# Performance work log

Measured on AMD Instinct MI355X. Metric: run time of the kernel, lower is better.

Reference implementation:

```python
import jax, jax.numpy as jnp
import numpy as np

N, D, E = 100000, 128, 800000

def setup_inputs() -> dict:
    key = jax.random.key(0)
    k1, k2, k3, k4 = jax.random.split(key, 4)
    z = jax.random.normal(k1, (N, D), dtype=jnp.float32)
    edge_index = jax.random.randint(k2, (2, E), 0, N, dtype=jnp.int64)
    # PyTorch-style init scale for Linear layers (kaiming-uniform-ish via normal is fine for a numeric reference)
    W1 = jax.random.normal(k3, (2 * D, D), dtype=jnp.float32) * (1.0 / np.sqrt(2 * D))
    b1 = jnp.zeros((D,), dtype=jnp.float32)
    W2 = jax.random.normal(k4, (D, 1), dtype=jnp.float32) * (1.0 / np.sqrt(D))
    b2 = jnp.zeros((1,), dtype=jnp.float32)
    return {"z": z, "edge_index": edge_index, "W1": W1, "b1": b1, "W2": W2, "b2": b2}

def reference(z, edge_index, W1, b1, W2, b2):
    # row/col gather of node embeddings
    row, col = edge_index[0], edge_index[1]
    # cat([z[row], z[col]]) @ W1 == z[row] @ W1[:D] + z[col] @ W1[D:]
    # -> avoids materializing the [E, 2D] concatenated tensor
    d = z.shape[1]
    h = z[row] @ W1[:d] + z[col] @ W1[d:] + b1          # [E, D]
    h = jax.nn.relu(h)                                   # Dropout(0.1) is identity in eval mode
    out = h @ W2 + b2                                    # [E, 1]
    return out.squeeze(-1)                               # [E]
```

## Files before the change

### kernel.cpp

```cpp
#include <hip/hip_runtime.h>

#define DDIM 128

typedef __bf16 bf16x8 __attribute__((ext_vector_type(8)));
typedef float  floatx4 __attribute__((ext_vector_type(4)));

__global__ __launch_bounds__(256, 4) void precompute_uv_mfma_q8(
    const float* __restrict__ z, const float* __restrict__ W1,
    const float* __restrict__ b1,
    unsigned char* __restrict__ U8, unsigned char* __restrict__ V8,
    float* __restrict__ u_scale, float* __restrict__ v_scale,
    int N, int nchunks)
{
    __shared__ unsigned short WsF[32 * 64 * 8];

    const int t    = threadIdx.x;
    const int lane = t & 63;
    const int w    = t >> 6;
    const int half = blockIdx.x;
    unsigned char* __restrict__ dst8 = half ? V8 : U8;
    float*         __restrict__ dscl = half ? v_scale : u_scale;
    const float*   __restrict__ Wh   = W1 + (size_t)half * DDIM * DDIM;

    const int mrow = lane & 15;
    const int quad = lane >> 4;
    const int gy   = gridDim.y;

    float4 rx[8];
    auto issue_loads = [&](int ch) {
        int grow = ch * 64 + w * 16 + mrow;
        if (grow > N - 1) grow = N - 1;
        const float* zrow = z + (size_t)grow * DDIM;
        #pragma unroll
        for (int ks = 0; ks < 4; ++ks) {
            const int k0 = ks * 32 + quad * 8;
            rx[2 * ks]     = *(const float4*)(zrow + k0);
            rx[2 * ks + 1] = *(const float4*)(zrow + k0 + 4);
        }
    };

    if (blockIdx.y < nchunks) issue_loads(blockIdx.y);

    {
        const int nlow = lane & 15;
        const int kq   = (lane >> 4) & 3;
        #pragma unroll
        for (int i = 0; i < 8; ++i) {
            const int ntks = w + i * 4;
            const int nt = ntks >> 2, ks = ntks & 3;
            const int n  = nt * 16 + nlow;
            const int kb = ks * 32 + kq * 8;
            float f[8];
            #pragma unroll
            for (int j = 0; j < 8; ++j)
                f[j] = Wh[(kb + j) * DDIM + n];
            unsigned pk[4];
            #pragma unroll
            for (int j = 0; j < 4; ++j)
                asm("v_cvt_pk_bf16_f32 %0, %1, %2"
                    : "=v"(pk[j]) : "v"(f[2 * j]), "v"(f[2 * j + 1]));
            *(uint4*)&WsF[(ntks * 64 + lane) * 8] = *(const uint4*)pk;
        }
    }

    float bval[8];
    #pragma unroll
    for (int nt = 0; nt < 8; ++nt)
        bval[nt] = (half == 0) ? b1[nt * 16 + mrow] : 0.f;

    __syncthreads();

    for (int chunk = blockIdx.y; chunk < nchunks; chunk += gy) {
        bf16x8 afrag[4];
        #pragma unroll
        for (int ks = 0; ks < 4; ++ks) {
            const float4 x0 = rx[2 * ks];
            const float4 x1 = rx[2 * ks + 1];
            unsigned pk[4];
            asm("v_cvt_pk_bf16_f32 %0, %1, %2" : "=v"(pk[0]) : "v"(x0.x), "v"(x0.y));
            asm("v_cvt_pk_bf16_f32 %0, %1, %2" : "=v"(pk[1]) : "v"(x0.z), "v"(x0.w));
            asm("v_cvt_pk_bf16_f32 %0, %1, %2" : "=v"(pk[2]) : "v"(x1.x), "v"(x1.y));
            asm("v_cvt_pk_bf16_f32 %0, %1, %2" : "=v"(pk[3]) : "v"(x1.z), "v"(x1.w));
            afrag[ks] = __builtin_bit_cast(bf16x8, *(const uint4*)pk);
        }

        const int nxt = chunk + gy;
        if (nxt < nchunks) issue_loads(nxt);

        floatx4 acc[8];
        #pragma unroll
        for (int nt = 0; nt < 8; ++nt)
            acc[nt] = (floatx4){bval[nt], bval[nt], bval[nt], bval[nt]};

        #pragma unroll
        for (int ks = 0; ks < 4; ++ks) {
            #pragma unroll
            for (int nt = 0; nt < 8; ++nt) {
                const bf16x8 b = __builtin_bit_cast(bf16x8,
                    *(const uint4*)&WsF[((nt * 4 + ks) * 64 + lane) * 8]);
                acc[nt] = __builtin_amdgcn_mfma_f32_16x16x32_bf16(afrag[ks], b, acc[nt], 0, 0, 0);
            }
        }

        #pragma unroll
        for (int r = 0; r < 4; ++r) {
            float mx = fmaxf(
                fmaxf(fmaxf(fabsf(acc[0][r]), fabsf(acc[1][r])),
                      fmaxf(fabsf(acc[2][r]), fabsf(acc[3][r]))),
                fmaxf(fmaxf(fabsf(acc[4][r]), fabsf(acc[5][r])),
                      fmaxf(fabsf(acc[6][r]), fabsf(acc[7][r]))));
            #pragma unroll
            for (int m = 1; m < 16; m <<= 1)
                mx = fmaxf(mx, __shfl_xor(mx, m, 16));
            mx = fmaxf(mx, 1e-20f);
            const float inv = 127.f * __builtin_amdgcn_rcpf(mx);

            unsigned char bytes[8];
            #pragma unroll
            for (int nt = 0; nt < 8; ++nt) {
                const float fq = fmaf(acc[nt][r], inv, 12583040.0f);
                bytes[nt] = (unsigned char)(__builtin_bit_cast(unsigned, fq) & 0xffu);
            }
            const int grow = chunk * 64 + w * 16 + quad * 4 + r;
            if (grow < N) {
                *(uint2*)&dst8[(size_t)grow * DDIM + mrow * 8] =
                    *(const uint2*)bytes;
                if (mrow == 0) dscl[grow] = mx * (1.f / 127.f);
            }
        }
    }
}

__global__ __launch_bounds__(256) void edge_kernel_i8(
    const int* __restrict__ ei,
    const unsigned char* __restrict__ U8, const unsigned char* __restrict__ V8,
    const float* __restrict__ u_scale, const float* __restrict__ v_scale,
    const float* __restrict__ W2, const float* __restrict__ b2,
    float* __restrict__ out, int E)
{
    const int t  = threadIdx.x;
    const int p  = t & 15;
    const int g0 = (blockIdx.x * 16 + (t >> 4)) * 4;
    if (g0 >= E) return;

    float ww[8];
    #pragma unroll
    for (int j = 0; j < 8; ++j) ww[j] = W2[j * 16 + p];

    int rows[4], cols[4];
    if (g0 + 3 < E) {
        const int4 r4 = *(const int4*)(ei + g0);
        const int4 c4 = *(const int4*)(ei + (size_t)E + g0);
        rows[0]=r4.x; rows[1]=r4.y; rows[2]=r4.z; rows[3]=r4.w;
        cols[0]=c4.x; cols[1]=c4.y; cols[2]=c4.z; cols[3]=c4.w;
    } else {
        #pragma unroll
        for (int i = 0; i < 4; ++i) {
            const int gi = (g0 + i < E) ? (g0 + i) : (E - 1);
            rows[i] = ei[gi];
            cols[i] = ei[(size_t)E + gi];
        }
    }

    uint2 uu[4], vv[4];
    #pragma unroll
    for (int i = 0; i < 4; ++i)
        uu[i] = *(const uint2*)(U8 + (size_t)rows[i] * DDIM + p * 8);
    #pragma unroll
    for (int i = 0; i < 4; ++i)
        vv[i] = *(const uint2*)(V8 + (size_t)cols[i] * DDIM + p * 8);

    float su[4], sv[4];
    #pragma unroll
    for (int i = 0; i < 4; ++i) { su[i] = u_scale[rows[i]]; sv[i] = v_scale[cols[i]]; }

    const float bias = b2[0];

    float sres[4];
    #pragma unroll
    for (int i = 0; i < 4; ++i) {
        const unsigned ul = uu[i].x, uh = uu[i].y;
        const unsigned vl = vv[i].x, vh = vv[i].y;
        const float c = -128.f * (su[i] + sv[i]);
        float s = 0.f;
        #pragma unroll
        for (int j = 0; j < 4; ++j) {
            const float uf = (float)((ul >> (8 * j)) & 0xffu);
            const float vf = (float)((vl >> (8 * j)) & 0xffu);
            const float h  = fmaf(su[i], uf, fmaf(sv[i], vf, c));
            s = fmaf(fmaxf(h, 0.f), ww[j], s);
        }
        #pragma unroll
        for (int j = 0; j < 4; ++j) {
            const float uf = (float)((uh >> (8 * j)) & 0xffu);
            const float vf = (float)((vh >> (8 * j)) & 0xffu);
            const float h  = fmaf(su[i], uf, fmaf(sv[i], vf, c));
            s = fmaf(fmaxf(h, 0.f), ww[4 + j], s);
        }
        #pragma unroll
        for (int off = 8; off > 0; off >>= 1)
            s += __shfl_down(s, off, 16);
        sres[i] = s + bias;
    }

    if (p == 0) {
        if (g0 + 3 < E) {
            float4 o; o.x = sres[0]; o.y = sres[1]; o.z = sres[2]; o.w = sres[3];
            *(float4*)&out[g0] = o;
        } else {
            #pragma unroll
            for (int i = 0; i < 4; ++i)
                if (g0 + i < E) out[g0 + i] = sres[i];
        }
    }
}

__global__ __launch_bounds__(256) void edge_fused_fallback(
    const float* __restrict__ z, const int* __restrict__ ei,
    const float* __restrict__ W1, const float* __restrict__ b1,
    const float* __restrict__ W2, const float* __restrict__ b2,
    float* __restrict__ out, int N, int E)
{
    const int tid  = blockIdx.x * 256 + threadIdx.x;
    const int e    = tid >> 6;
    const int lane = tid & 63;
    if (e >= E) return;

    const int row = ei[e];
    const int col = ei[(size_t)E + e];
    const float* zr = z + (size_t)row * DDIM;
    const float* zc = z + (size_t)col * DDIM;

    float h0 = b1[lane];
    float h1 = b1[lane + 64];
    for (int k = 0; k < DDIM; ++k) {
        const float a = zr[k];
        const float b = zc[k];
        h0 = fmaf(a, W1[k * DDIM + lane],               h0);
        h0 = fmaf(b, W1[(DDIM + k) * DDIM + lane],      h0);
        h1 = fmaf(a, W1[k * DDIM + lane + 64],          h1);
        h1 = fmaf(b, W1[(DDIM + k) * DDIM + lane + 64], h1);
    }
    float s = fmaxf(h0, 0.f) * W2[lane] + fmaxf(h1, 0.f) * W2[lane + 64];
    #pragma unroll
    for (int off = 32; off > 0; off >>= 1)
        s += __shfl_down(s, off, 64);
    if (lane == 0) out[e] = s + b2[0];
}

extern "C" void kernel_launch(void* const* d_in, const int* in_sizes, int n_in,
                              void* d_out, int out_size, void* d_ws, size_t ws_size,
                              hipStream_t stream)
{
    const float* z  = (const float*)d_in[0];
    const int*   ei = (const int*)d_in[1];
    const float* W1 = (const float*)d_in[2];
    const float* b1 = (const float*)d_in[3];
    const float* W2 = (const float*)d_in[4];
    const float* b2 = (const float*)d_in[5];
    float*       out = (float*)d_out;

    const int N = in_sizes[0] / DDIM;
    const int E = in_sizes[1] / 2;

    const size_t n128 = (size_t)N * DDIM;
    const size_t need = 2 * n128 + 2 * (size_t)N * sizeof(float) + 256;
    if (ws_size >= need) {
        unsigned char* U8 = (unsigned char*)d_ws;
        unsigned char* V8 = U8 + n128;
        float* usc = (float*)(((size_t)(V8 + n128) + 255) & ~(size_t)255);
        float* vsc = usc + N;
        const int nchunks = (N + 63) / 64;
        const int gy = (nchunks + 1) / 2;
        hipLaunchKernelGGL(precompute_uv_mfma_q8, dim3(2, gy), dim3(256), 0, stream,
                           z, W1, b1, U8, V8, usc, vsc, N, nchunks);
        hipLaunchKernelGGL(edge_kernel_i8, dim3((E + 63) / 64), dim3(256), 0, stream,
                           ei, U8, V8, usc, vsc, W2, b2, out, E);
    } else {
        hipLaunchKernelGGL(edge_fused_fallback, dim3((E + 3) / 4), dim3(256), 0, stream,
                           z, ei, W1, b1, W2, b2, out, N, E);
    }
}
```

Measured before the change: 140.1 us.

## Compute both U and V halves per block to reuse z row loads

Merges the two grid halves of the precompute kernel so each block stages both halves of W1 in shared memory (doubling LDS to 64KB) and computes both the U and V projections from a single load of each z chunk. This halves global reads of z and halves the block count. In exchange, per-block LDS use doubles and the W1 staging work per block doubles, which may reduce occupancy.

New measurement: 140.0 us. No clear change (-0.0%).

```diff
diff --git a/kernel.cpp b/kernel.cpp
--- a/kernel.cpp
+++ b/kernel.cpp
@@ -12,19 +12,14 @@
     float* __restrict__ u_scale, float* __restrict__ v_scale,
     int N, int nchunks)
 {
-    __shared__ unsigned short WsF[32 * 64 * 8];
+    __shared__ unsigned short WsF[2 * 32 * 64 * 8];
 
     const int t    = threadIdx.x;
     const int lane = t & 63;
     const int w    = t >> 6;
-    const int half = blockIdx.x;
-    unsigned char* __restrict__ dst8 = half ? V8 : U8;
-    float*         __restrict__ dscl = half ? v_scale : u_scale;
-    const float*   __restrict__ Wh   = W1 + (size_t)half * DDIM * DDIM;
-
     const int mrow = lane & 15;
     const int quad = lane >> 4;
-    const int gy   = gridDim.y;
+    const int gy   = gridDim.x;
 
     float4 rx[8];
     auto issue_loads = [&](int ch) {
@@ -39,17 +34,20 @@
         }
     };
 
-    if (blockIdx.y < nchunks) issue_loads(blockIdx.y);
+    issue_loads(blockIdx.x);
 
     {
         const int nlow = lane & 15;
         const int kq   = (lane >> 4) & 3;
-        #pragma unroll
-        for (int i = 0; i < 8; ++i) {
-            const int ntks = w + i * 4;
+        #pragma unroll 4
+        for (int i = 0; i < 16; ++i) {
+            const int s    = w + i * 4;
+            const int half = s >> 5;
+            const int ntks = s & 31;
             const int nt = ntks >> 2, ks = ntks & 3;
             const int n  = nt * 16 + nlow;
             const int kb = ks * 32 + kq * 8;
+            const float* __restrict__ Wh = W1 + (size_t)half * DDIM * DDIM;
             float f[8];
             #pragma unroll
             for (int j = 0; j < 8; ++j)
@@ -59,18 +57,18 @@
             for (int j = 0; j < 4; ++j)
                 asm("v_cvt_pk_bf16_f32 %0, %1, %2"
                     : "=v"(pk[j]) : "v"(f[2 * j]), "v"(f[2 * j + 1]));
-            *(uint4*)&WsF[(ntks * 64 + lane) * 8] = *(const uint4*)pk;
+            *(uint4*)&WsF[(s * 64 + lane) * 8] = *(const uint4*)pk;
         }
     }
 
     float bval[8];
     #pragma unroll
     for (int nt = 0; nt < 8; ++nt)
-        bval[nt] = (half == 0) ? b1[nt * 16 + mrow] : 0.f;
+        bval[nt] = b1[nt * 16 + mrow];
 
     __syncthreads();
 
-    for (int chunk = blockIdx.y; chunk < nchunks; chunk += gy) {
+    for (int chunk = blockIdx.x; chunk < nchunks; chunk += gy) {
         bf16x8 afrag[4];
         #pragma unroll
         for (int ks = 0; ks < 4; ++ks) {
@@ -87,45 +85,54 @@
         const int nxt = chunk + gy;
         if (nxt < nchunks) issue_loads(nxt);
 
-        floatx4 acc[8];
-        #pragma unroll
-        for (int nt = 0; nt < 8; ++nt)
-            acc[nt] = (floatx4){bval[nt], bval[nt], bval[nt], bval[nt]};
-
-        #pragma unroll
-        for (int ks = 0; ks < 4; ++ks) {
+        #pragma unroll
+        for (int h = 0; h < 2; ++h) {
+            unsigned char* __restrict__ dst8 = h ? V8 : U8;
+            float*         __restrict__ dscl = h ? v_scale : u_scale;
+
+            floatx4 acc[8];
             #pragma unroll
             for (int nt = 0; nt < 8; ++nt) {
-                const bf16x8 b = __builtin_bit_cast(bf16x8,
-                    *(const uint4*)&WsF[((nt * 4 + ks) * 64 + lane) * 8]);
-                acc[nt] = __builtin_amdgcn_mfma_f32_16x16x32_bf16(afrag[ks], b, acc[nt], 0, 0, 0);
+                const float b0 = h ? 0.f : bval[nt];
+                acc[nt] = (floatx4){b0, b0, b0, b0};
             }
-        }
-
-        #pragma unroll
-        for (int r = 0; r < 4; ++r) {
-            float mx = fmaxf(
-                fmaxf(fmaxf(fabsf(acc[0][r]), fabsf(acc[1][r])),
-                      fmaxf(fabsf(acc[2][r]), fabsf(acc[3][r]))),
-                fmaxf(fmaxf(fabsf(acc[4][r]), fabsf(acc[5][r])),
-                      fmaxf(fabsf(acc[6][r]), fabsf(acc[7][r]))));
-            #pragma unroll
-            for (int m = 1; m < 16; m <<= 1)
-                mx = fmaxf(mx, __shfl_xor(mx, m, 16));
-            mx = fmaxf(mx, 1e-20f);
-            const float inv = 127.f * __builtin_amdgcn_rcpf(mx);
-
-            unsigned char bytes[8];
-            #pragma unroll
-            for (int nt = 0; nt < 8; ++nt) {
-                const float fq = fmaf(acc[nt][r], inv, 12583040.0f);
-                bytes[nt] = (unsigned char)(__builtin_bit_cast(unsigned, fq) & 0xffu);
+
+            #pragma unroll
+            for (int ks = 0; ks < 4; ++ks) {
+                #pragma unroll
+                for (int nt = 0; nt < 8; ++nt) {
+                    const bf16x8 b = __builtin_bit_cast(bf16x8,
+                        *(const uint4*)&WsF[((h * 32 + nt * 4 + ks) * 64 + lane) * 8]);
+                    acc[nt] = __builtin_amdgcn_mfma_f32_16x16x32_bf16(
+                        afrag[ks], b, acc[nt], 0, 0, 0);
+                }
             }
-            const int grow = chunk * 64 + w * 16 + quad * 4 + r;
-            if (grow < N) {
-                *(uint2*)&dst8[(size_t)grow * DDIM + mrow * 8] =
-                    *(const uint2*)bytes;
-                if (mrow == 0) dscl[grow] = mx * (1.f / 127.f);
+
+            #pragma unroll
+            for (int r = 0; r < 4; ++r) {
+                float mx = fmaxf(
+                    fmaxf(fmaxf(fabsf(acc[0][r]), fabsf(acc[1][r])),
+                          fmaxf(fabsf(acc[2][r]), fabsf(acc[3][r]))),
+                    fmaxf(fmaxf(fabsf(acc[4][r]), fabsf(acc[5][r])),
+                          fmaxf(fabsf(acc[6][r]), fabsf(acc[7][r]))));
+                #pragma unroll
+                for (int m = 1; m < 16; m <<= 1)
+                    mx = fmaxf(mx, __shfl_xor(mx, m, 16));
+                mx = fmaxf(mx, 1e-20f);
+                const float inv = 127.f * __builtin_amdgcn_rcpf(mx);
+
+                unsigned char bytes[8];
+                #pragma unroll
+                for (int nt = 0; nt < 8; ++nt) {
+                    const float fq = fmaf(acc[nt][r], inv, 12583040.0f);
+                    bytes[nt] = (unsigned char)(__builtin_bit_cast(unsigned, fq) & 0xffu);
+                }
+                const int grow = chunk * 64 + w * 16 + quad * 4 + r;
+                if (grow < N) {
+                    *(uint2*)&dst8[(size_t)grow * DDIM + mrow * 8] =
+                        *(const uint2*)bytes;
+                    if (mrow == 0) dscl[grow] = mx * (1.f / 127.f);
+                }
             }
         }
     }
@@ -272,7 +279,7 @@
         float* vsc = usc + N;
         const int nchunks = (N + 63) / 64;
         const int gy = (nchunks + 1) / 2;
-        hipLaunchKernelGGL(precompute_uv_mfma_q8, dim3(2, gy), dim3(256), 0, stream,
+        hipLaunchKernelGGL(precompute_uv_mfma_q8, dim3(gy), dim3(256), 0, stream,
                            z, W1, b1, U8, V8, usc, vsc, N, nchunks);
         hipLaunchKernelGGL(edge_kernel_i8, dim3((E + 63) / 64), dim3(256), 0, stream,
                            ei, U8, V8, usc, vsc, W2, b2, out, E);
```
